# Optimization experiments

Measured on AMD Instinct MI355X. Metric: run time of the kernel, lower is better.

Reference implementation:

```python
import jax, jax.numpy as jnp
import numpy as np

B, S, D, N = 8, 4096, 768, 64


def setup_inputs() -> dict:
    key = jax.random.key(0)
    k1, k2 = jax.random.split(key)
    word_vectors = jax.random.normal(k1, (B, S, D), dtype=jnp.float32)
    sent_rep_token_ids = jnp.sort(jax.random.randint(k2, (B, N), 0, S), axis=1)
    sent_rep_mask = jnp.ones((B, N), dtype=jnp.float32)
    # sent_lengths: each row must sum exactly to S (torch.split contract).
    rng = np.random.default_rng(0)
    lens = np.stack([
        np.diff(np.concatenate([[0], np.sort(rng.choice(np.arange(1, S), N - 1, replace=False)), [S]]))
        for _ in range(B)
    ])
    sent_lengths = jnp.asarray(lens, dtype=jnp.int64) if jax.config.jax_enable_x64 else jnp.asarray(lens, dtype=jnp.int32)
    sent_lengths_mask = jnp.ones((B, N), dtype=jnp.float32)
    return {
        "word_vectors": word_vectors,
        "sent_rep_token_ids": sent_rep_token_ids,
        "sent_rep_mask": sent_rep_mask,
        "sent_lengths": sent_lengths,
        "sent_lengths_mask": sent_lengths_mask,
    }


def reference(word_vectors, sent_rep_token_ids, sent_rep_mask, sent_lengths, sent_lengths_mask):
    b, s, d = word_vectors.shape
    n = sent_lengths.shape[1]
    dt = word_vectors.dtype

    # --- sent_rep_tokens branch: gather CLS-style token per sentence ---
    rep_vec = jnp.take_along_axis(word_vectors, sent_rep_token_ids[:, :, None], axis=1)  # [B,N,D]
    rep_vec = rep_vec * sent_rep_mask[:, :, None].astype(dt)

    # --- mean_tokens branch: ragged per-segment mean via segment_sum ---
    ends = jnp.cumsum(sent_lengths, axis=1)                      # [B,N] exclusive-end offsets
    pos = jnp.arange(s)
    seg = jax.vmap(lambda e: jnp.searchsorted(e, pos, side='right'))(ends)  # [B,S] segment id per token
    gseg = (seg + jnp.arange(b)[:, None] * n).reshape(-1)        # global segment ids [B*S]
    flat = word_vectors.reshape(b * s, d)
    sums = jax.ops.segment_sum(flat, gseg, num_segments=b * n).reshape(b, n, d)
    counts = jax.ops.segment_sum((flat != 0).astype(dt), gseg, num_segments=b * n).reshape(b, n, d)
    mean = sums / jnp.maximum(counts, 1)
    # fallback to word_vectors[0,0] when a segment has zero nonzero entries (original semantics)
    all_zero = (counts.sum(axis=-1) == 0)                        # [B,N]
    mean = jnp.where(all_zero[:, :, None], word_vectors[0, 0], mean)
    mean_vec = mean * sent_lengths_mask[:, :, None].astype(dt)

    out_vectors = jnp.concatenate([rep_vec, mean_vec], axis=1)   # [B,2N,D]
    out_masks = jnp.concatenate([sent_rep_mask, sent_lengths_mask], axis=1)  # [B,2N]
    return out_vectors, out_masks
```

## Files before the change

### kernel.cpp

```cpp
#include <hip/hip_runtime.h>

#define BB 8
#define SS 4096
#define DD 768
#define NN 64
#define D4 (DD / 4)
#define WAVES 8
#define BLOCK (WAVES * 64)

__global__ __launch_bounds__(BLOCK) void pool_kernel(
    const float* __restrict__ wv,
    const int* __restrict__ rep_ids,
    const float* __restrict__ rep_mask,
    const int* __restrict__ lens,
    const float* __restrict__ len_mask,
    float* __restrict__ out)
{
    __shared__ float4 s_sum[WAVES][64];
    __shared__ float4 s_cnt[WAVES][64];

    const int seg  = blockIdx.x;
    const int g    = blockIdx.y;
    const int b    = seg >> 6;
    const int n    = seg & 63;
    const int tid  = threadIdx.x;
    const int lane = tid & 63;
    const int w    = tid >> 6;

    int myLen = lens[b * NN + lane];
    int pre   = (lane < n) ? myLen : 0;
    #pragma unroll
    for (int off = 32; off; off >>= 1) pre += __shfl_xor(pre, off);
    const int start = pre;
    const int len   = __shfl(myLen, n);

    const int col4 = g * 64 + lane;
    const float4* wv4 = (const float4*)wv;
    const float4* p   = wv4 + ((size_t)(b * SS + start) + w) * D4 + col4;

    float4 sum = make_float4(0.f, 0.f, 0.f, 0.f);
    float4 cnt = make_float4(0.f, 0.f, 0.f, 0.f);
    #pragma unroll 8
    for (int t = w; t < len; t += WAVES) {
        float4 v = *p;
        p += (size_t)WAVES * D4;
        sum.x += v.x; sum.y += v.y; sum.z += v.z; sum.w += v.w;
        cnt.x += (v.x != 0.f) ? 1.f : 0.f;
        cnt.y += (v.y != 0.f) ? 1.f : 0.f;
        cnt.z += (v.z != 0.f) ? 1.f : 0.f;
        cnt.w += (v.w != 0.f) ? 1.f : 0.f;
    }

    s_sum[w][lane] = sum;
    s_cnt[w][lane] = cnt;
    __syncthreads();

    if (w == 0) {
        float4 S = make_float4(0.f, 0.f, 0.f, 0.f);
        float4 C = make_float4(0.f, 0.f, 0.f, 0.f);
        #pragma unroll
        for (int j = 0; j < WAVES; ++j) {
            float4 a = s_sum[j][lane];
            float4 c = s_cnt[j][lane];
            S.x += a.x; S.y += a.y; S.z += a.z; S.w += a.w;
            C.x += c.x; C.y += c.y; C.z += c.z; C.w += c.w;
        }

        float4 mean;
        mean.x = S.x / fmaxf(C.x, 1.f);
        mean.y = S.y / fmaxf(C.y, 1.f);
        mean.z = S.z / fmaxf(C.z, 1.f);
        mean.w = S.w / fmaxf(C.w, 1.f);

        float tot = C.x + C.y + C.z + C.w;
        unsigned long long nz = __ballot(tot != 0.f);
        if (nz == 0ULL) {
            mean = wv4[col4];
        }

        const float lm = len_mask[b * NN + n];
        mean.x *= lm; mean.y *= lm; mean.z *= lm; mean.w *= lm;

        float4* out4 = (float4*)out;
        out4[(size_t)(b * 2 * NN + NN + n) * D4 + col4] = mean;

        const int   rid = rep_ids[b * NN + n];
        const float rm  = rep_mask[b * NN + n];
        float4 rv = wv4[(size_t)(b * SS + rid) * D4 + col4];
        rv.x *= rm; rv.y *= rm; rv.z *= rm; rv.w *= rm;
        out4[(size_t)(b * 2 * NN + n) * D4 + col4] = rv;

        if (g == 0 && lane == 0) {
            float* masks = out + (size_t)BB * 2 * NN * DD;
            masks[b * 2 * NN + n]      = rm;
            masks[b * 2 * NN + NN + n] = lm;
        }
    }
}

extern "C" void kernel_launch(void* const* d_in, const int* in_sizes, int n_in,
                              void* d_out, int out_size, void* d_ws, size_t ws_size,
                              hipStream_t stream) {
    const float* wv       = (const float*)d_in[0];
    const int*   rep_ids  = (const int*)d_in[1];
    const float* rep_mask = (const float*)d_in[2];
    const int*   lens     = (const int*)d_in[3];
    const float* len_mask = (const float*)d_in[4];
    float*       out      = (float*)d_out;

    dim3 grid(BB * NN, 3);
    pool_kernel<<<grid, BLOCK, 0, stream>>>(wv, rep_ids, rep_mask, lens, len_mask, out);
}
```

Baseline: 159.0 us.

## Split segment mean into fixed token tiles with atomic partial sums and finalize pass

Replaces the one-block-per-segment reduction, whose work varies with segment length, with equal-size token tiles per batch. Each wave accumulates its 16 tokens over the full 768-wide row and flushes partial sums and counts to a zeroed workspace with float atomics at segment boundaries. A separate finalize kernel computes the mean, the fallback and the rep gather. The aim is to remove load imbalance from ragged segments. In exchange it adds two extra launches, a workspace zeroing pass, many global atomics, and a summation order that is no longer deterministic.

```diff
diff --git a/kernel.cpp b/kernel.cpp
--- a/kernel.cpp
+++ b/kernel.cpp
@@ -5,92 +5,141 @@
 #define DD 768
 #define NN 64
 #define D4 (DD / 4)
-#define WAVES 8
-#define BLOCK (WAVES * 64)
+#define TT 64
+#define TPW 16
+#define NTILES (SS / TT)
+#define WS_N (BB * NN * DD)
 
-__global__ __launch_bounds__(BLOCK) void pool_kernel(
+__global__ __launch_bounds__(256) void zero_ws(float4* ws4) {
+    int i = blockIdx.x * 256 + threadIdx.x;
+    ws4[i] = make_float4(0.f, 0.f, 0.f, 0.f);
+}
+
+__global__ __launch_bounds__(256) void partial_kernel(
     const float* __restrict__ wv,
-    const int* __restrict__ rep_ids,
-    const float* __restrict__ rep_mask,
     const int* __restrict__ lens,
-    const float* __restrict__ len_mask,
-    float* __restrict__ out)
+    float* __restrict__ ws_sum,
+    float* __restrict__ ws_cnt)
 {
-    __shared__ float4 s_sum[WAVES][64];
-    __shared__ float4 s_cnt[WAVES][64];
-
-    const int seg  = blockIdx.x;
-    const int g    = blockIdx.y;
-    const int b    = seg >> 6;
-    const int n    = seg & 63;
+    __shared__ int s_ends[NN];
+    const int b    = blockIdx.x >> 6;
+    const int tile = blockIdx.x & (NTILES - 1);
     const int tid  = threadIdx.x;
     const int lane = tid & 63;
     const int w    = tid >> 6;
 
-    int myLen = lens[b * NN + lane];
-    int pre   = (lane < n) ? myLen : 0;
-    #pragma unroll
-    for (int off = 32; off; off >>= 1) pre += __shfl_xor(pre, off);
-    const int start = pre;
-    const int len   = __shfl(myLen, n);
-
-    const int col4 = g * 64 + lane;
-    const float4* wv4 = (const float4*)wv;
-    const float4* p   = wv4 + ((size_t)(b * SS + start) + w) * D4 + col4;
-
-    float4 sum = make_float4(0.f, 0.f, 0.f, 0.f);
-    float4 cnt = make_float4(0.f, 0.f, 0.f, 0.f);
-    #pragma unroll 8
-    for (int t = w; t < len; t += WAVES) {
-        float4 v = *p;
-        p += (size_t)WAVES * D4;
-        sum.x += v.x; sum.y += v.y; sum.z += v.z; sum.w += v.w;
-        cnt.x += (v.x != 0.f) ? 1.f : 0.f;
-        cnt.y += (v.y != 0.f) ? 1.f : 0.f;
-        cnt.z += (v.z != 0.f) ? 1.f : 0.f;
-        cnt.w += (v.w != 0.f) ? 1.f : 0.f;
+    if (tid < NN) {
+        int l = lens[b * NN + tid];
+        #pragma unroll
+        for (int off = 1; off < 64; off <<= 1) {
+            int v = __shfl_up(l, off);
+            if (lane >= off) l += v;
+        }
+        s_ends[tid] = l;
     }
-
-    s_sum[w][lane] = sum;
-    s_cnt[w][lane] = cnt;
     __syncthreads();
 
-    if (w == 0) {
-        float4 S = make_float4(0.f, 0.f, 0.f, 0.f);
-        float4 C = make_float4(0.f, 0.f, 0.f, 0.f);
-        #pragma unroll
-        for (int j = 0; j < WAVES; ++j) {
-            float4 a = s_sum[j][lane];
-            float4 c = s_cnt[j][lane];
-            S.x += a.x; S.y += a.y; S.z += a.z; S.w += a.w;
-            C.x += c.x; C.y += c.y; C.z += c.z; C.w += c.w;
+    const int t0 = tile * TT + w * TPW;
+    int lo = 0, hi = NN - 1;
+    while (lo < hi) { int mid = (lo + hi) >> 1; if (s_ends[mid] > t0) hi = mid; else lo = mid + 1; }
+    int seg    = lo;
+    int segend = s_ends[seg];
+
+    const float4* row = (const float4*)wv + (size_t)(b * SS + t0) * D4;
+    float4 s0 = make_float4(0,0,0,0), s1 = s0, s2 = s0;
+    float4 c0 = s0, c1 = s0, c2 = s0;
+
+    auto flush = [&](int sg) {
+        float* ps = ws_sum + (size_t)(b * NN + sg) * DD;
+        float* pc = ws_cnt + (size_t)(b * NN + sg) * DD;
+        const int c = lane * 4;
+        atomicAdd(ps + c + 0, s0.x); atomicAdd(ps + c + 1, s0.y);
+        atomicAdd(ps + c + 2, s0.z); atomicAdd(ps + c + 3, s0.w);
+        atomicAdd(ps + 256 + c + 0, s1.x); atomicAdd(ps + 256 + c + 1, s1.y);
+        atomicAdd(ps + 256 + c + 2, s1.z); atomicAdd(ps + 256 + c + 3, s1.w);
+        atomicAdd(ps + 512 + c + 0, s2.x); atomicAdd(ps + 512 + c + 1, s2.y);
+        atomicAdd(ps + 512 + c + 2, s2.z); atomicAdd(ps + 512 + c + 3, s2.w);
+        atomicAdd(pc + c + 0, c0.x); atomicAdd(pc + c + 1, c0.y);
+        atomicAdd(pc + c + 2, c0.z); atomicAdd(pc + c + 3, c0.w);
+        atomicAdd(pc + 256 + c + 0, c1.x); atomicAdd(pc + 256 + c + 1, c1.y);
+        atomicAdd(pc + 256 + c + 2, c1.z); atomicAdd(pc + 256 + c + 3, c1.w);
+        atomicAdd(pc + 512 + c + 0, c2.x); atomicAdd(pc + 512 + c + 1, c2.y);
+        atomicAdd(pc + 512 + c + 2, c2.z); atomicAdd(pc + 512 + c + 3, c2.w);
+    };
+
+    #pragma unroll 4
+    for (int tok = 0; tok < TPW; ++tok) {
+        const int t = t0 + tok;
+        if (t >= segend) {
+            flush(seg);
+            s0 = s1 = s2 = c0 = c1 = c2 = make_float4(0,0,0,0);
+            do { ++seg; segend = s_ends[seg]; } while (t >= segend);
         }
+        float4 v0 = row[lane];
+        float4 v1 = row[64 + lane];
+        float4 v2 = row[128 + lane];
+        row += D4;
+        s0.x += v0.x; s0.y += v0.y; s0.z += v0.z; s0.w += v0.w;
+        s1.x += v1.x; s1.y += v1.y; s1.z += v1.z; s1.w += v1.w;
+        s2.x += v2.x; s2.y += v2.y; s2.z += v2.z; s2.w += v2.w;
+        c0.x += (v0.x != 0.f) ? 1.f : 0.f; c0.y += (v0.y != 0.f) ? 1.f : 0.f;
+        c0.z += (v0.z != 0.f) ? 1.f : 0.f; c0.w += (v0.w != 0.f) ? 1.f : 0.f;
+        c1.x += (v1.x != 0.f) ? 1.f : 0.f; c1.y += (v1.y != 0.f) ? 1.f : 0.f;
+        c1.z += (v1.z != 0.f) ? 1.f : 0.f; c1.w += (v1.w != 0.f) ? 1.f : 0.f;
+        c2.x += (v2.x != 0.f) ? 1.f : 0.f; c2.y += (v2.y != 0.f) ? 1.f : 0.f;
+        c2.z += (v2.z != 0.f) ? 1.f : 0.f; c2.w += (v2.w != 0.f) ? 1.f : 0.f;
+    }
+    flush(seg);
+}
 
+__global__ __launch_bounds__(256) void finalize_kernel(
+    const float* __restrict__ wv,
+    const int* __restrict__ rep_ids,
+    const float* __restrict__ rep_mask,
+    const float* __restrict__ len_mask,
+    const float* __restrict__ ws_sum,
+    const float* __restrict__ ws_cnt,
+    float* __restrict__ out)
+{
+    __shared__ float s_part[4];
+    const int sgid = blockIdx.x;
+    const int b = sgid >> 6, n = sgid & 63;
+    const int tid = threadIdx.x;
+    const bool active = tid < D4;
+
+    const float4* sum4 = (const float4*)ws_sum + (size_t)sgid * D4;
+    const float4* cnt4 = (const float4*)ws_cnt + (size_t)sgid * D4;
+    float4 S = make_float4(0,0,0,0), C = S;
+    if (active) { S = sum4[tid]; C = cnt4[tid]; }
+
+    float tot = C.x + C.y + C.z + C.w;
+    #pragma unroll
+    for (int off = 32; off; off >>= 1) tot += __shfl_xor(tot, off);
+    if ((tid & 63) == 0) s_part[tid >> 6] = tot;
+    __syncthreads();
+    const float total = s_part[0] + s_part[1] + s_part[2] + s_part[3];
+
+    if (active) {
         float4 mean;
         mean.x = S.x / fmaxf(C.x, 1.f);
         mean.y = S.y / fmaxf(C.y, 1.f);
         mean.z = S.z / fmaxf(C.z, 1.f);
         mean.w = S.w / fmaxf(C.w, 1.f);
+        if (total == 0.f) mean = ((const float4*)wv)[tid];
 
-        float tot = C.x + C.y + C.z + C.w;
-        unsigned long long nz = __ballot(tot != 0.f);
-        if (nz == 0ULL) {
-            mean = wv4[col4];
-        }
-
-        const float lm = len_mask[b * NN + n];
+        const float lm = len_mask[sgid];
         mean.x *= lm; mean.y *= lm; mean.z *= lm; mean.w *= lm;
 
         float4* out4 = (float4*)out;
-        out4[(size_t)(b * 2 * NN + NN + n) * D4 + col4] = mean;
+        out4[(size_t)(b * 2 * NN + NN + n) * D4 + tid] = mean;
 
-        const int   rid = rep_ids[b * NN + n];
-        const float rm  = rep_mask[b * NN + n];
-        float4 rv = wv4[(size_t)(b * SS + rid) * D4 + col4];
+        const int   rid = rep_ids[sgid];
+        const float rm  = rep_mask[sgid];
+        float4 rv = ((const float4*)wv)[(size_t)(b * SS + rid) * D4 + tid];
         rv.x *= rm; rv.y *= rm; rv.z *= rm; rv.w *= rm;
-        out4[(size_t)(b * 2 * NN + n) * D4 + col4] = rv;
+        out4[(size_t)(b * 2 * NN + n) * D4 + tid] = rv;
 
-        if (g == 0 && lane == 0) {
+        if (tid == 0) {
             float* masks = out + (size_t)BB * 2 * NN * DD;
             masks[b * 2 * NN + n]      = rm;
             masks[b * 2 * NN + NN + n] = lm;
@@ -107,7 +156,11 @@
     const int*   lens     = (const int*)d_in[3];
     const float* len_mask = (const float*)d_in[4];
     float*       out      = (float*)d_out;
+    float*       ws_sum   = (float*)d_ws;
+    float*       ws_cnt   = ws_sum + WS_N;
 
-    dim3 grid(BB * NN, 3);
-    pool_kernel<<<grid, BLOCK, 0, stream>>>(wv, rep_ids, rep_mask, lens, len_mask, out);
+    zero_ws<<<(2 * WS_N / 4) / 256, 256, 0, stream>>>((float4*)d_ws);
+    partial_kernel<<<BB * NTILES, 256, 0, stream>>>(wv, lens, ws_sum, ws_cnt);
+    finalize_kernel<<<BB * NN, 256, 0, stream>>>(wv, rep_ids, rep_mask, len_mask,
+                                                 ws_sum, ws_cnt, out);
 }
```

New measurement: 197.5 us. +24.2%, slower.
